# Performance work log

Hardware: AMD Instinct MI355X
Metric: run time of the kernel (lower is better)

Reference implementation:

```python
import jax, jax.numpy as jnp
from jax import lax
import numpy as np

H = 256

def _cell(x, h, c, wih, whh, bih, bhh):
    # PyTorch LSTMCell: gates ordered i, f, g, o
    g = x @ wih.T + bih + h @ whh.T + bhh
    i, f, gg, o = jnp.split(g, 4, axis=-1)
    c = jax.nn.sigmoid(f) * c + jax.nn.sigmoid(i) * jnp.tanh(gg)
    h = jax.nn.sigmoid(o) * jnp.tanh(c)
    return h, c


def setup_inputs() -> dict:
    key = jax.random.key(0)
    ks = iter(jax.random.split(key, 64))
    def lin(out_f, in_f):
        s = 1.0 / np.sqrt(in_f)
        w = jax.random.uniform(next(ks), (out_f, in_f), minval=-s, maxval=s, dtype=jnp.float32)
        b = jax.random.uniform(next(ks), (out_f,), minval=-s, maxval=s, dtype=jnp.float32)
        return w, b
    def cellp():
        s = 1.0 / np.sqrt(H)
        return tuple(jax.random.uniform(next(ks), sh, minval=-s, maxval=s, dtype=jnp.float32)
                     for sh in [(4 * H, H), (4 * H, H), (4 * H,), (4 * H,)])
    d = {}
    d['x'] = jax.random.normal(next(ks), (20, 256, 64, 64), dtype=jnp.float32)
    d['fc_en1_w'], d['fc_en1_b'] = lin(1024, 4096)
    d['fc_en2_w'], d['fc_en2_b'] = lin(H, 1024)
    for nm in ['en1', 'en2', 'en3', 'de1', 'de2', 'de3']:
        d[nm + '_wih'], d[nm + '_whh'], d[nm + '_bih'], d[nm + '_bhh'] = cellp()
    d['fc_de1_w'], d['fc_de1_b'] = lin(1024, H)
    d['fc_de2_w'], d['fc_de2_b'] = lin(4096, 1024)
    d['future_step'] = 10
    return d


def reference(x, fc_en1_w, fc_en1_b, fc_en2_w, fc_en2_b,
              en1_wih, en1_whh, en1_bih, en1_bhh,
              en2_wih, en2_whh, en2_bih, en2_bhh,
              en3_wih, en3_whh, en3_bih, en3_bhh,
              de1_wih, de1_whh, de1_bih, de1_bhh,
              de2_wih, de2_whh, de2_bih, de2_bhh,
              de3_wih, de3_whh, de3_bih, de3_bhh,
              fc_de1_w, fc_de1_b, fc_de2_w, fc_de2_b, future_step):
    seq, B = x.shape[0], x.shape[1]
    xf = x.reshape(seq, B, -1)  # (S, B, 4096)
    z0 = jnp.zeros((B, H), x.dtype)

    def enc_step(carry, xt):
        h1, c1, h2, c2, h3, c3 = carry
        z = jax.nn.relu(xt @ fc_en1_w.T + fc_en1_b)
        z = jax.nn.relu(z @ fc_en2_w.T + fc_en2_b)
        h1, c1 = _cell(z, h1, c1, en1_wih, en1_whh, en1_bih, en1_bhh)
        h2, c2 = _cell(h1, h2, c2, en2_wih, en2_whh, en2_bih, en2_bhh)
        h3, c3 = _cell(h2, h3, c3, en3_wih, en3_whh, en3_bih, en3_bhh)
        return (h1, c1, h2, c2, h3, c3), None

    enc_carry, _ = lax.scan(enc_step, (z0,) * 6, xf)
    h_e3 = enc_carry[4]

    def dec_step(carry, _):
        h1, c1, h2, c2, h3, c3 = carry
        h1, c1 = _cell(z0, h1, c1, de1_wih, de1_whh, de1_bih, de1_bhh)
        h2, c2 = _cell(h1, h2, c2, de2_wih, de2_whh, de2_bih, de2_bhh)
        h3, c3 = _cell(h2, h3, c3, de3_wih, de3_whh, de3_bih, de3_bhh)
        y = jax.nn.relu(h3 @ fc_de1_w.T + fc_de1_b)
        y = jnp.tanh(y @ fc_de2_w.T + fc_de2_b)
        return (h1, c1, h2, c2, h3, c3), y

    _, ys = lax.scan(dec_step, (h_e3, z0, z0, z0, z0, z0), None, length=future_step)
    return ys.reshape(future_step, B, 64, 64)
```

## Files before the change

### kernel.cpp

```cpp
#include <hip/hip_runtime.h>
#include <math.h>

static __device__ __forceinline__ float sigf(float v) { return 1.0f / (1.0f + expf(-v)); }

using s8v = __attribute__((ext_vector_type(8))) short;
using f4v = __attribute__((ext_vector_type(4))) float;

static __device__ __forceinline__ void splitf(float f, unsigned short& h, unsigned short& l) {
  unsigned u = __float_as_uint(f);
  unsigned short hb = (unsigned short)((u + 0x7FFFu + ((u >> 16) & 1u)) >> 16);
  float hf = __uint_as_float(((unsigned)hb) << 16);
  float lf = f - hf;
  unsigned ul = __float_as_uint(lf);
  unsigned short lb = (unsigned short)((ul + 0x7FFFu + ((ul >> 16) & 1u)) >> 16);
  h = hb; l = lb;
}

static __device__ __forceinline__ void splitf4(float4 a, uint2& hOut, uint2& lOut) {
  unsigned hxy, hzw;
  asm("v_cvt_pk_bf16_f32 %0, %1, %2" : "=v"(hxy) : "v"(a.x), "v"(a.y));
  asm("v_cvt_pk_bf16_f32 %0, %1, %2" : "=v"(hzw) : "v"(a.z), "v"(a.w));
  float hx = __uint_as_float(hxy << 16);
  float hy = __uint_as_float(hxy & 0xFFFF0000u);
  float hz = __uint_as_float(hzw << 16);
  float hw = __uint_as_float(hzw & 0xFFFF0000u);
  unsigned lxy, lzw;
  asm("v_cvt_pk_bf16_f32 %0, %1, %2" : "=v"(lxy) : "v"(a.x - hx), "v"(a.y - hy));
  asm("v_cvt_pk_bf16_f32 %0, %1, %2" : "=v"(lzw) : "v"(a.z - hz), "v"(a.w - hw));
  hOut.x = hxy; hOut.y = hzw;
  lOut.x = lxy; lOut.y = lzw;
}

__global__ __launch_bounds__(256) void wsplit(
    const float* __restrict__ W, unsigned short* __restrict__ WH,
    unsigned short* __restrict__ WL, int n4)
{
  int i = blockIdx.x * 256 + threadIdx.x;
  if (i < n4) {
    float4 v = ((const float4*)W)[i];
    ushort4 h, l;
    splitf(v.x, h.x, l.x); splitf(v.y, h.y, l.y);
    splitf(v.z, h.z, l.z); splitf(v.w, h.w, l.w);
    ((ushort4*)WH)[i] = h;
    ((ushort4*)WL)[i] = l;
  }
}

template <int OSPLIT>
__global__ __launch_bounds__(256) void gemm_sf(
    const float* __restrict__ A,
    const unsigned short* __restrict__ WH, const unsigned short* __restrict__ WL,
    const float* __restrict__ bias, float* __restrict__ C,
    unsigned short* __restrict__ OH, unsigned short* __restrict__ OL,
    int M, int N, int K, int act)
{
  __shared__ unsigned short AsH[128 * 40];
  __shared__ unsigned short AsL[128 * 40];
  __shared__ unsigned short WsH[64 * 40];
  __shared__ unsigned short WsL[64 * 40];

  const int t = threadIdx.x;
  const int w = t >> 6, lane = t & 63;
  const int lrow = lane & 15, lk = (lane >> 4) * 8;
  const int m0 = blockIdx.x * 128, n0 = blockIdx.y * 64;

  f4v acc[2][4];
#pragma unroll
  for (int i = 0; i < 2; ++i)
#pragma unroll
    for (int j = 0; j < 4; ++j) acc[i][j] = (f4v){0.f, 0.f, 0.f, 0.f};

  for (int k0 = 0; k0 < K; k0 += 32) {
#pragma unroll
    for (int i = 0; i < 4; ++i) {
      int v = i * 256 + t;
      int row = v >> 3, kq = (v & 7) << 2;
      float4 a = *(const float4*)(A + (size_t)(m0 + row) * K + k0 + kq);
      uint2 h2, l2;
      splitf4(a, h2, l2);
      *(uint2*)&AsH[row * 40 + kq] = h2;
      *(uint2*)&AsL[row * 40 + kq] = l2;
    }
    {
      int row = t >> 2, q = (t & 3) * 8;
      *(s8v*)&WsH[row * 40 + q] = *(const s8v*)(WH + (size_t)(n0 + row) * K + k0 + q);
      *(s8v*)&WsL[row * 40 + q] = *(const s8v*)(WL + (size_t)(n0 + row) * K + k0 + q);
    }
    __syncthreads();

    s8v aH[2], aL[2], bH[4], bL[4];
#pragma unroll
    for (int mt = 0; mt < 2; ++mt) {
      int r = (w * 32 + mt * 16 + lrow) * 40 + lk;
      aH[mt] = *(const s8v*)&AsH[r];
      aL[mt] = *(const s8v*)&AsL[r];
    }
#pragma unroll
    for (int nt = 0; nt < 4; ++nt) {
      int r = (nt * 16 + lrow) * 40 + lk;
      bH[nt] = *(const s8v*)&WsH[r];
      bL[nt] = *(const s8v*)&WsL[r];
    }
#pragma unroll
    for (int mt = 0; mt < 2; ++mt)
#pragma unroll
      for (int nt = 0; nt < 4; ++nt) {
        acc[mt][nt] = __builtin_amdgcn_mfma_f32_16x16x32_bf16(aH[mt], bH[nt], acc[mt][nt], 0, 0, 0);
        acc[mt][nt] = __builtin_amdgcn_mfma_f32_16x16x32_bf16(aH[mt], bL[nt], acc[mt][nt], 0, 0, 0);
        acc[mt][nt] = __builtin_amdgcn_mfma_f32_16x16x32_bf16(aL[mt], bH[nt], acc[mt][nt], 0, 0, 0);
      }
    __syncthreads();
  }

#pragma unroll
  for (int mt = 0; mt < 2; ++mt)
#pragma unroll
    for (int nt = 0; nt < 4; ++nt) {
      int gcol = n0 + nt * 16 + lrow;
      float bv = bias[gcol];
#pragma unroll
      for (int r = 0; r < 4; ++r) {
        int grow = m0 + w * 32 + mt * 16 + (lane >> 4) * 4 + r;
        float v = acc[mt][nt][r] + bv;
        if (act == 1) v = fmaxf(v, 0.f);
        else if (act == 2) v = tanhf(v);
        if (OSPLIT) {
          unsigned short h, l;
          splitf(v, h, l);
          OH[(size_t)grow * N + gcol] = h;
          OL[(size_t)grow * N + gcol] = l;
        } else {
          C[(size_t)grow * N + gcol] = v;
        }
      }
    }
}

template <int OSPLIT>
__global__ __launch_bounds__(256) void gemm_bb(
    const unsigned short* __restrict__ AH, const unsigned short* __restrict__ AL,
    const unsigned short* __restrict__ WH, const unsigned short* __restrict__ WL,
    const float* __restrict__ bias, float* __restrict__ C,
    unsigned short* __restrict__ OH, unsigned short* __restrict__ OL,
    int M, int N, int K, int act)
{
  __shared__ unsigned short AsH[128 * 40];
  __shared__ unsigned short AsL[128 * 40];
  __shared__ unsigned short WsH[64 * 40];
  __shared__ unsigned short WsL[64 * 40];

  const int t = threadIdx.x;
  const int w = t >> 6, lane = t & 63;
  const int lrow = lane & 15, lk = (lane >> 4) * 8;
  const int m0 = blockIdx.x * 128, n0 = blockIdx.y * 64;

  f4v acc[2][4];
#pragma unroll
  for (int i = 0; i < 2; ++i)
#pragma unroll
    for (int j = 0; j < 4; ++j) acc[i][j] = (f4v){0.f, 0.f, 0.f, 0.f};

  for (int k0 = 0; k0 < K; k0 += 32) {
#pragma unroll
    for (int i = 0; i < 2; ++i) {
      int v = i * 256 + t;
      int row = v >> 2, q = (v & 3) * 8;
      *(s8v*)&AsH[row * 40 + q] = *(const s8v*)(AH + (size_t)(m0 + row) * K + k0 + q);
      *(s8v*)&AsL[row * 40 + q] = *(const s8v*)(AL + (size_t)(m0 + row) * K + k0 + q);
    }
    {
      int row = t >> 2, q = (t & 3) * 8;
      *(s8v*)&WsH[row * 40 + q] = *(const s8v*)(WH + (size_t)(n0 + row) * K + k0 + q);
      *(s8v*)&WsL[row * 40 + q] = *(const s8v*)(WL + (size_t)(n0 + row) * K + k0 + q);
    }
    __syncthreads();

    s8v aH[2], aL[2], bH[4], bL[4];
#pragma unroll
    for (int mt = 0; mt < 2; ++mt) {
      int r = (w * 32 + mt * 16 + lrow) * 40 + lk;
      aH[mt] = *(const s8v*)&AsH[r];
      aL[mt] = *(const s8v*)&AsL[r];
    }
#pragma unroll
    for (int nt = 0; nt < 4; ++nt) {
      int r = (nt * 16 + lrow) * 40 + lk;
      bH[nt] = *(const s8v*)&WsH[r];
      bL[nt] = *(const s8v*)&WsL[r];
    }
#pragma unroll
    for (int mt = 0; mt < 2; ++mt)
#pragma unroll
      for (int nt = 0; nt < 4; ++nt) {
        acc[mt][nt] = __builtin_amdgcn_mfma_f32_16x16x32_bf16(aH[mt], bH[nt], acc[mt][nt], 0, 0, 0);
        acc[mt][nt] = __builtin_amdgcn_mfma_f32_16x16x32_bf16(aH[mt], bL[nt], acc[mt][nt], 0, 0, 0);
        acc[mt][nt] = __builtin_amdgcn_mfma_f32_16x16x32_bf16(aL[mt], bH[nt], acc[mt][nt], 0, 0, 0);
      }
    __syncthreads();
  }

#pragma unroll
  for (int mt = 0; mt < 2; ++mt)
#pragma unroll
    for (int nt = 0; nt < 4; ++nt) {
      int gcol = n0 + nt * 16 + lrow;
      float bv = bias[gcol];
#pragma unroll
      for (int r = 0; r < 4; ++r) {
        int grow = m0 + w * 32 + mt * 16 + (lane >> 4) * 4 + r;
        float v = acc[mt][nt][r] + bv;
        if (act == 1) v = fmaxf(v, 0.f);
        else if (act == 2) v = tanhf(v);
        if (OSPLIT) {
          unsigned short h, l;
          splitf(v, h, l);
          OH[(size_t)grow * N + gcol] = h;
          OL[(size_t)grow * N + gcol] = l;
        } else {
          C[(size_t)grow * N + gcol] = v;
        }
      }
    }
}

__global__ __launch_bounds__(256) void prep_pack(
    const float* __restrict__ wih, const float* __restrict__ whh,
    const float* __restrict__ bih, const float* __restrict__ bhh,
    float* __restrict__ wihP, float* __restrict__ whhP, float* __restrict__ bP)
{
  const int j = blockIdx.x, k = threadIdx.x;
  float4 a, c;
  a.x = wih[(0 * 256 + j) * 256 + k];
  a.y = wih[(1 * 256 + j) * 256 + k];
  a.z = wih[(2 * 256 + j) * 256 + k];
  a.w = wih[(3 * 256 + j) * 256 + k];
  *(float4*)&wihP[((size_t)j * 256 + k) * 4] = a;
  c.x = whh[(0 * 256 + j) * 256 + k];
  c.y = whh[(1 * 256 + j) * 256 + k];
  c.z = whh[(2 * 256 + j) * 256 + k];
  c.w = whh[(3 * 256 + j) * 256 + k];
  *(float4*)&whhP[((size_t)j * 256 + k) * 4] = c;
  if (k < 4) bP[j * 4 + k] = bih[k * 256 + j] + bhh[k * 256 + j];
}

__global__ __launch_bounds__(256) void transpose256(
    const float* __restrict__ in, float* __restrict__ out)
{
  const int t = blockIdx.x, c4 = blockIdx.y;
  const int r = threadIdx.x;
  float4 v = *(const float4*)(in + ((size_t)t * 256 + r) * 256 + c4 * 4);
  float* op = out + (size_t)t * 65536 + (size_t)(c4 * 4) * 256 + r;
  op[0]   = v.x;
  op[256] = v.y;
  op[512] = v.z;
  op[768] = v.w;
}

__global__ __launch_bounds__(256) void transpose256s(
    const float* __restrict__ in, unsigned short* __restrict__ outH,
    unsigned short* __restrict__ outL)
{
  const int t = blockIdx.x, c4 = blockIdx.y;
  const int r = threadIdx.x;
  float4 v = *(const float4*)(in + ((size_t)t * 256 + r) * 256 + c4 * 4);
  ushort4 h, l;
  splitf(v.x, h.x, l.x); splitf(v.y, h.y, l.y);
  splitf(v.z, h.z, l.z); splitf(v.w, h.w, l.w);
  size_t o = (size_t)t * 65536 + (size_t)(c4 * 4) * 256 + r;
  outH[o] = h.x; outH[o + 256] = h.y; outH[o + 512] = h.z; outH[o + 768] = h.w;
  outL[o] = l.x; outL[o + 256] = l.y; outL[o + 512] = l.z; outL[o + 768] = l.w;
}

struct CellSlot {
  const float* x;
  const float* wih;
  const float* whh;
  const float* bias;
  const float* hin;
  float* c;
  float* hout;
  float* hcopy;
  int hasx;
};
struct CellArgs { CellSlot s[3]; };

__global__ __launch_bounds__(512) void cell_multi(CellArgs args)
{
  __shared__ float part[4][64][4];
  const CellSlot S = args.s[blockIdx.x >> 8];
  const int inner = blockIdx.x & 255;
  const int jg = inner & 63, bg = inner >> 6;
  const int t = threadIdx.x;
  const int lane = t & 63;
  const int wave = t >> 6;
  const int jwv = wave & 3;
  const int kh = __builtin_amdgcn_readfirstlane(wave >> 2);
  const int b = bg * 64 + lane;

  const int jw = __builtin_amdgcn_readfirstlane(jg * 4 + jwv);
  const float4* wh = (const float4*)(S.whh + (size_t)jw * 1024) + kh * 128;
  const float4* wi = (const float4*)(S.wih + (size_t)jw * 1024) + kh * 128;
  const float* hcol = S.hin + (size_t)kh * 128 * 256 + b;

  float4 acc;
  if (kh == 0) acc = *(const float4*)(S.bias + jw * 4);
  else         acc = (float4){0.f, 0.f, 0.f, 0.f};

  if (S.hasx) {
    const float* xcol = S.x + (size_t)kh * 128 * 256 + b;
#pragma unroll 8
    for (int k = 0; k < 128; ++k) {
      const float hv = hcol[k * 256];
      const float4 wv = wh[k];
      acc.x = fmaf(hv, wv.x, acc.x);
      acc.y = fmaf(hv, wv.y, acc.y);
      acc.z = fmaf(hv, wv.z, acc.z);
      acc.w = fmaf(hv, wv.w, acc.w);
      const float xv = xcol[k * 256];
      const float4 vv = wi[k];
      acc.x = fmaf(xv, vv.x, acc.x);
      acc.y = fmaf(xv, vv.y, acc.y);
      acc.z = fmaf(xv, vv.z, acc.z);
      acc.w = fmaf(xv, vv.w, acc.w);
    }
  } else {
#pragma unroll 8
    for (int k = 0; k < 128; ++k) {
      const float hv = hcol[k * 256];
      const float4 wv = wh[k];
      acc.x = fmaf(hv, wv.x, acc.x);
      acc.y = fmaf(hv, wv.y, acc.y);
      acc.z = fmaf(hv, wv.z, acc.z);
      acc.w = fmaf(hv, wv.w, acc.w);
    }
  }

  if (kh == 1) *(float4*)&part[jwv][lane][0] = acc;
  __syncthreads();
  if (kh == 0) {
    const float4 p = *(const float4*)&part[jwv][lane][0];
    acc.x += p.x; acc.y += p.y; acc.z += p.z; acc.w += p.w;

    const int idx = jw * 256 + b;
    const float cold = S.c[idx];
    const float ig = sigf(acc.x), fg = sigf(acc.y);
    const float gg = tanhf(acc.z), og = sigf(acc.w);
    const float cn = fg * cold + ig * gg;
    const float hn = og * tanhf(cn);
    S.c[idx] = cn;
    S.hout[idx] = hn;
    if (S.hcopy) S.hcopy[idx] = hn;
  }
}


extern "C" void kernel_launch(void* const* d_in, const int* in_sizes, int n_in,
                              void* d_out, int out_size, void* d_ws, size_t ws_size,
                              hipStream_t stream)
{
  const float* x_in  = (const float*)d_in[0];
  const float* w_en1 = (const float*)d_in[1];
  const float* b_en1 = (const float*)d_in[2];
  const float* w_en2 = (const float*)d_in[3];
  const float* b_en2 = (const float*)d_in[4];
  const float* cw[6][4];
  for (int i = 0; i < 6; ++i)
    for (int j = 0; j < 4; ++j) cw[i][j] = (const float*)d_in[5 + i * 4 + j];
  const float* w_de1 = (const float*)d_in[29];
  const float* b_de1 = (const float*)d_in[30];
  const float* w_de2 = (const float*)d_in[31];
  const float* b_de2 = (const float*)d_in[32];
  float* out = (float*)d_out;

  float* fs   = (float*)d_ws;
  float* wihP = fs;
  float* whhP = wihP + 6 * 262144;
  float* bP   = whhP + 6 * 262144;
  float* hb   = bP + 6 * 1024;
  float* cb   = hb + 12 * 65536;
  float* H3T  = cb + 6 * 65536;
  float* z2   = H3T + 10 * 65536;
  float* z2T  = z2 + 1310720;
  unsigned short* us = (unsigned short*)(z2T + 1310720);
  unsigned short* WEN1H = us;              us += 4194304;
  unsigned short* WEN1L = us;              us += 4194304;
  unsigned short* WEN2H = us;              us += 262144;
  unsigned short* WEN2L = us;              us += 262144;
  unsigned short* WDE1H = us;              us += 262144;
  unsigned short* WDE1L = us;              us += 262144;
  unsigned short* WDE2H = us;              us += 4194304;
  unsigned short* WDE2L = us;              us += 4194304;
  unsigned short* Z1H   = us;              us += 5242880;
  unsigned short* Z1L   = us;              us += 5242880;
  unsigned short* H3H = Z1H;
  unsigned short* H3L = Z1H + 655360;
  unsigned short* Y1H = Z1H + 1310720;
  unsigned short* Y1L = Z1H + 1310720 + 2621440;

  for (int i = 0; i < 6; ++i)
    prep_pack<<<256, 256, 0, stream>>>(cw[i][0], cw[i][1], cw[i][2], cw[i][3],
                                       wihP + i * 262144, whhP + i * 262144,
                                       bP + i * 1024);
  wsplit<<<4096, 256, 0, stream>>>(w_en1, WEN1H, WEN1L, 1048576);
  wsplit<<<256, 256, 0, stream>>>(w_en2, WEN2H, WEN2L, 65536);
  wsplit<<<256, 256, 0, stream>>>(w_de1, WDE1H, WDE1L, 65536);
  wsplit<<<4096, 256, 0, stream>>>(w_de2, WDE2H, WDE2L, 1048576);
  hipMemsetAsync(hb, 0, (size_t)18 * 65536 * sizeof(float), stream);

  gemm_sf<1><<<dim3(40, 16), 256, 0, stream>>>(
      x_in, WEN1H, WEN1L, b_en1, nullptr, Z1H, Z1L, 5120, 1024, 4096, 1);
  gemm_bb<0><<<dim3(40, 4), 256, 0, stream>>>(
      Z1H, Z1L, WEN2H, WEN2L, b_en2, z2, nullptr, nullptr, 5120, 256, 1024, 1);
  transpose256<<<dim3(20, 64), 256, 0, stream>>>(z2, z2T);

  int pp[6] = {0, 0, 0, 0, 0, 0};
  auto HBuf = [&](int l, int p) { return hb + (size_t)(l * 2 + p) * 65536; };
  auto CBuf = [&](int l) { return cb + (size_t)l * 65536; };
  auto WI = [&](int l) { return wihP + (size_t)l * 262144; };
  auto WHp = [&](int l) { return whhP + (size_t)l * 262144; };
  auto BB = [&](int l) { return bP + (size_t)l * 1024; };

  for (int s = 0; s <= 21; ++s) {
    CellArgs a; int n = 0; int tog[3]; int nt = 0;
    if (s < 20) {
      a.s[n++] = {z2T + (size_t)s * 65536, WI(0), WHp(0), BB(0),
                  HBuf(0, pp[0]), CBuf(0), HBuf(0, pp[0] ^ 1), nullptr, 1};
      tog[nt++] = 0;
    }
    if (s >= 1 && s <= 20) {
      a.s[n++] = {HBuf(0, pp[0]), WI(1), WHp(1), BB(1),
                  HBuf(1, pp[1]), CBuf(1), HBuf(1, pp[1] ^ 1), nullptr, 1};
      tog[nt++] = 1;
    }
    if (s >= 2) {
      a.s[n++] = {HBuf(1, pp[1]), WI(2), WHp(2), BB(2),
                  HBuf(2, pp[2]), CBuf(2), HBuf(2, pp[2] ^ 1), nullptr, 1};
      tog[nt++] = 2;
    }
    cell_multi<<<n * 256, 512, 0, stream>>>(a);
    for (int i = 0; i < nt; ++i) pp[tog[i]] ^= 1;
  }

  for (int s = 0; s <= 11; ++s) {
    CellArgs a; int n = 0; int tog[3]; int nt = 0;
    if (s < 10) {
      const float* h1in = (s == 0) ? HBuf(2, pp[2]) : HBuf(3, pp[3]);
      a.s[n++] = {nullptr, WI(3), WHp(3), BB(3),
                  h1in, CBuf(3), HBuf(3, pp[3] ^ 1), nullptr, 0};
      tog[nt++] = 3;
    }
    if (s >= 1 && s <= 10) {
      a.s[n++] = {HBuf(3, pp[3]), WI(4), WHp(4), BB(4),
                  HBuf(4, pp[4]), CBuf(4), HBuf(4, pp[4] ^ 1), nullptr, 1};
      tog[nt++] = 4;
    }
    if (s >= 2) {
      a.s[n++] = {HBuf(4, pp[4]), WI(5), WHp(5), BB(5),
                  HBuf(5, pp[5]), CBuf(5), HBuf(5, pp[5] ^ 1),
                  H3T + (size_t)(s - 2) * 65536, 1};
      tog[nt++] = 5;
    }
    cell_multi<<<n * 256, 512, 0, stream>>>(a);
    for (int i = 0; i < nt; ++i) pp[tog[i]] ^= 1;
  }

  transpose256s<<<dim3(10, 64), 256, 0, stream>>>(H3T, H3H, H3L);
  gemm_bb<1><<<dim3(20, 16), 256, 0, stream>>>(
      H3H, H3L, WDE1H, WDE1L, b_de1, nullptr, Y1H, Y1L, 2560, 1024, 256, 1);
  gemm_bb<0><<<dim3(20, 64), 256, 0, stream>>>(
      Y1H, Y1L, WDE2H, WDE2L, b_de2, out, nullptr, nullptr, 2560, 4096, 1024, 2);

  (void)in_sizes; (void)n_in; (void)out_size; (void)ws_size;
}
```

Baseline: 854.7 us.

## Retile fp32-input GEMM to 64x128 and batch weight-prep kernel launches

The first encoder GEMM, which reads fp32 activations and splits them into bf16 hi/lo pairs, now uses 64-row by 128-column tiles instead of 128x64. Each fp32 activation element is therefore split fewer times across column blocks, while each wave keeps a wider strip of 8 accumulators. The six LSTM weight-pack launches are merged into one 2D-grid launch, and the four weight-split launches into one segmented launch, to cut launch overhead. The trade-off is more reads of the weight operand per tile, more registers per wave, and a different grid shape (80x8).

```diff
diff --git a/kernel.cpp b/kernel.cpp
--- a/kernel.cpp
+++ b/kernel.cpp
@@ -31,19 +31,26 @@
   lOut.x = lxy; lOut.y = lzw;
 }
 
-__global__ __launch_bounds__(256) void wsplit(
-    const float* __restrict__ W, unsigned short* __restrict__ WH,
-    unsigned short* __restrict__ WL, int n4)
-{
-  int i = blockIdx.x * 256 + threadIdx.x;
-  if (i < n4) {
-    float4 v = ((const float4*)W)[i];
-    ushort4 h, l;
-    splitf(v.x, h.x, l.x); splitf(v.y, h.y, l.y);
-    splitf(v.z, h.z, l.z); splitf(v.w, h.w, l.w);
-    ((ushort4*)WH)[i] = h;
-    ((ushort4*)WL)[i] = l;
-  }
+struct WsplitArgs {
+  const float* W[4];
+  unsigned short* WH[4];
+  unsigned short* WL[4];
+};
+__global__ __launch_bounds__(256) void wsplit4(WsplitArgs a)
+{
+  int blk = blockIdx.x;
+  int seg, base;
+  if (blk < 4096)      { seg = 0; base = blk; }
+  else if (blk < 4352) { seg = 1; base = blk - 4096; }
+  else if (blk < 4608) { seg = 2; base = blk - 4352; }
+  else                 { seg = 3; base = blk - 4608; }
+  int i = base * 256 + threadIdx.x;
+  float4 v = ((const float4*)a.W[seg])[i];
+  ushort4 h, l;
+  splitf(v.x, h.x, l.x); splitf(v.y, h.y, l.y);
+  splitf(v.z, h.z, l.z); splitf(v.w, h.w, l.w);
+  ((ushort4*)a.WH[seg])[i] = h;
+  ((ushort4*)a.WL[seg])[i] = l;
 }
 
 template <int OSPLIT>
@@ -54,25 +61,23 @@
     unsigned short* __restrict__ OH, unsigned short* __restrict__ OL,
     int M, int N, int K, int act)
 {
-  __shared__ unsigned short AsH[128 * 40];
-  __shared__ unsigned short AsL[128 * 40];
-  __shared__ unsigned short WsH[64 * 40];
-  __shared__ unsigned short WsL[64 * 40];
+  __shared__ unsigned short AsH[64 * 40];
+  __shared__ unsigned short AsL[64 * 40];
+  __shared__ unsigned short WsH[128 * 40];
+  __shared__ unsigned short WsL[128 * 40];
 
   const int t = threadIdx.x;
   const int w = t >> 6, lane = t & 63;
   const int lrow = lane & 15, lk = (lane >> 4) * 8;
-  const int m0 = blockIdx.x * 128, n0 = blockIdx.y * 64;
-
-  f4v acc[2][4];
-#pragma unroll
-  for (int i = 0; i < 2; ++i)
-#pragma unroll
-    for (int j = 0; j < 4; ++j) acc[i][j] = (f4v){0.f, 0.f, 0.f, 0.f};
+  const int m0 = blockIdx.x * 64, n0 = blockIdx.y * 128;
+
+  f4v acc[8];
+#pragma unroll
+  for (int j = 0; j < 8; ++j) acc[j] = (f4v){0.f, 0.f, 0.f, 0.f};
 
   for (int k0 = 0; k0 < K; k0 += 32) {
 #pragma unroll
-    for (int i = 0; i < 4; ++i) {
+    for (int i = 0; i < 2; ++i) {
       int v = i * 256 + t;
       int row = v >> 3, kq = (v & 7) << 2;
       float4 a = *(const float4*)(A + (size_t)(m0 + row) * K + k0 + kq);
@@ -80,6 +85,90 @@
       splitf4(a, h2, l2);
       *(uint2*)&AsH[row * 40 + kq] = h2;
       *(uint2*)&AsL[row * 40 + kq] = l2;
+    }
+#pragma unroll
+    for (int i = 0; i < 2; ++i) {
+      int v = i * 256 + t;
+      int row = v >> 2, q = (v & 3) * 8;
+      *(s8v*)&WsH[row * 40 + q] = *(const s8v*)(WH + (size_t)(n0 + row) * K + k0 + q);
+      *(s8v*)&WsL[row * 40 + q] = *(const s8v*)(WL + (size_t)(n0 + row) * K + k0 + q);
+    }
+    __syncthreads();
+
+    s8v aH, aL, bH[8], bL[8];
+    {
+      int r = (w * 16 + lrow) * 40 + lk;
+      aH = *(const s8v*)&AsH[r];
+      aL = *(const s8v*)&AsL[r];
+    }
+#pragma unroll
+    for (int nt = 0; nt < 8; ++nt) {
+      int r = (nt * 16 + lrow) * 40 + lk;
+      bH[nt] = *(const s8v*)&WsH[r];
+      bL[nt] = *(const s8v*)&WsL[r];
+    }
+#pragma unroll
+    for (int nt = 0; nt < 8; ++nt) {
+      acc[nt] = __builtin_amdgcn_mfma_f32_16x16x32_bf16(aH, bH[nt], acc[nt], 0, 0, 0);
+      acc[nt] = __builtin_amdgcn_mfma_f32_16x16x32_bf16(aH, bL[nt], acc[nt], 0, 0, 0);
+      acc[nt] = __builtin_amdgcn_mfma_f32_16x16x32_bf16(aL, bH[nt], acc[nt], 0, 0, 0);
+    }
+    __syncthreads();
+  }
+
+#pragma unroll
+  for (int nt = 0; nt < 8; ++nt) {
+    int gcol = n0 + nt * 16 + lrow;
+    float bv = bias[gcol];
+#pragma unroll
+    for (int r = 0; r < 4; ++r) {
+      int grow = m0 + w * 16 + (lane >> 4) * 4 + r;
+      float v = acc[nt][r] + bv;
+      if (act == 1) v = fmaxf(v, 0.f);
+      else if (act == 2) v = tanhf(v);
+      if (OSPLIT) {
+        unsigned short h, l;
+        splitf(v, h, l);
+        OH[(size_t)grow * N + gcol] = h;
+        OL[(size_t)grow * N + gcol] = l;
+      } else {
+        C[(size_t)grow * N + gcol] = v;
+      }
+    }
+  }
+}
+
+template <int OSPLIT>
+__global__ __launch_bounds__(256) void gemm_bb(
+    const unsigned short* __restrict__ AH, const unsigned short* __restrict__ AL,
+    const unsigned short* __restrict__ WH, const unsigned short* __restrict__ WL,
+    const float* __restrict__ bias, float* __restrict__ C,
+    unsigned short* __restrict__ OH, unsigned short* __restrict__ OL,
+    int M, int N, int K, int act)
+{
+  __shared__ unsigned short AsH[128 * 40];
+  __shared__ unsigned short AsL[128 * 40];
+  __shared__ unsigned short WsH[64 * 40];
+  __shared__ unsigned short WsL[64 * 40];
+
+  const int t = threadIdx.x;
+  const int w = t >> 6, lane = t & 63;
+  const int lrow = lane & 15, lk = (lane >> 4) * 8;
+  const int m0 = blockIdx.x * 128, n0 = blockIdx.y * 64;
+
+  f4v acc[2][4];
+#pragma unroll
+  for (int i = 0; i < 2; ++i)
+#pragma unroll
+    for (int j = 0; j < 4; ++j) acc[i][j] = (f4v){0.f, 0.f, 0.f, 0.f};
+
+  for (int k0 = 0; k0 < K; k0 += 32) {
+#pragma unroll
+    for (int i = 0; i < 2; ++i) {
+      int v = i * 256 + t;
+      int row = v >> 2, q = (v & 3) * 8;
+      *(s8v*)&AsH[row * 40 + q] = *(const s8v*)(AH + (size_t)(m0 + row) * K + k0 + q);
+      *(s8v*)&AsL[row * 40 + q] = *(const s8v*)(AL + (size_t)(m0 + row) * K + k0 + q);
     }
     {
       int row = t >> 2, q = (t & 3) * 8;
@@ -136,111 +225,36 @@
     }
 }
 
-template <int OSPLIT>
-__global__ __launch_bounds__(256) void gemm_bb(
-    const unsigned short* __restrict__ AH, const unsigned short* __restrict__ AL,
-    const unsigned short* __restrict__ WH, const unsigned short* __restrict__ WL,
-    const float* __restrict__ bias, float* __restrict__ C,
-    unsigned short* __restrict__ OH, unsigned short* __restrict__ OL,
-    int M, int N, int K, int act)
-{
-  __shared__ unsigned short AsH[128 * 40];
-  __shared__ unsigned short AsL[128 * 40];
-  __shared__ unsigned short WsH[64 * 40];
-  __shared__ unsigned short WsL[64 * 40];
-
-  const int t = threadIdx.x;
-  const int w = t >> 6, lane = t & 63;
-  const int lrow = lane & 15, lk = (lane >> 4) * 8;
-  const int m0 = blockIdx.x * 128, n0 = blockIdx.y * 64;
-
-  f4v acc[2][4];
-#pragma unroll
-  for (int i = 0; i < 2; ++i)
-#pragma unroll
-    for (int j = 0; j < 4; ++j) acc[i][j] = (f4v){0.f, 0.f, 0.f, 0.f};
-
-  for (int k0 = 0; k0 < K; k0 += 32) {
-#pragma unroll
-    for (int i = 0; i < 2; ++i) {
-      int v = i * 256 + t;
-      int row = v >> 2, q = (v & 3) * 8;
-      *(s8v*)&AsH[row * 40 + q] = *(const s8v*)(AH + (size_t)(m0 + row) * K + k0 + q);
-      *(s8v*)&AsL[row * 40 + q] = *(const s8v*)(AL + (size_t)(m0 + row) * K + k0 + q);
-    }
-    {
-      int row = t >> 2, q = (t & 3) * 8;
-      *(s8v*)&WsH[row * 40 + q] = *(const s8v*)(WH + (size_t)(n0 + row) * K + k0 + q);
-      *(s8v*)&WsL[row * 40 + q] = *(const s8v*)(WL + (size_t)(n0 + row) * K + k0 + q);
-    }
-    __syncthreads();
-
-    s8v aH[2], aL[2], bH[4], bL[4];
-#pragma unroll
-    for (int mt = 0; mt < 2; ++mt) {
-      int r = (w * 32 + mt * 16 + lrow) * 40 + lk;
-      aH[mt] = *(const s8v*)&AsH[r];
-      aL[mt] = *(const s8v*)&AsL[r];
-    }
-#pragma unroll
-    for (int nt = 0; nt < 4; ++nt) {
-      int r = (nt * 16 + lrow) * 40 + lk;
-      bH[nt] = *(const s8v*)&WsH[r];
-      bL[nt] = *(const s8v*)&WsL[r];
-    }
-#pragma unroll
-    for (int mt = 0; mt < 2; ++mt)
-#pragma unroll
-      for (int nt = 0; nt < 4; ++nt) {
-        acc[mt][nt] = __builtin_amdgcn_mfma_f32_16x16x32_bf16(aH[mt], bH[nt], acc[mt][nt], 0, 0, 0);
-        acc[mt][nt] = __builtin_amdgcn_mfma_f32_16x16x32_bf16(aH[mt], bL[nt], acc[mt][nt], 0, 0, 0);
-        acc[mt][nt] = __builtin_amdgcn_mfma_f32_16x16x32_bf16(aL[mt], bH[nt], acc[mt][nt], 0, 0, 0);
-      }
-    __syncthreads();
-  }
-
-#pragma unroll
-  for (int mt = 0; mt < 2; ++mt)
-#pragma unroll
-    for (int nt = 0; nt < 4; ++nt) {
-      int gcol = n0 + nt * 16 + lrow;
-      float bv = bias[gcol];
-#pragma unroll
-      for (int r = 0; r < 4; ++r) {
-        int grow = m0 + w * 32 + mt * 16 + (lane >> 4) * 4 + r;
-        float v = acc[mt][nt][r] + bv;
-        if (act == 1) v = fmaxf(v, 0.f);
-        else if (act == 2) v = tanhf(v);
-        if (OSPLIT) {
-          unsigned short h, l;
-          splitf(v, h, l);
-          OH[(size_t)grow * N + gcol] = h;
-          OL[(size_t)grow * N + gcol] = l;
-        } else {
-          C[(size_t)grow * N + gcol] = v;
-        }
-      }
-    }
-}
-
-__global__ __launch_bounds__(256) void prep_pack(
-    const float* __restrict__ wih, const float* __restrict__ whh,
-    const float* __restrict__ bih, const float* __restrict__ bhh,
-    float* __restrict__ wihP, float* __restrict__ whhP, float* __restrict__ bP)
-{
+struct PrepArgs {
+  const float* wih[6];
+  const float* whh[6];
+  const float* bih[6];
+  const float* bhh[6];
+  float* wihP;
+  float* whhP;
+  float* bP;
+};
+__global__ __launch_bounds__(256) void prep_pack6(PrepArgs a)
+{
+  const int l = blockIdx.y;
   const int j = blockIdx.x, k = threadIdx.x;
-  float4 a, c;
-  a.x = wih[(0 * 256 + j) * 256 + k];
-  a.y = wih[(1 * 256 + j) * 256 + k];
-  a.z = wih[(2 * 256 + j) * 256 + k];
-  a.w = wih[(3 * 256 + j) * 256 + k];
-  *(float4*)&wihP[((size_t)j * 256 + k) * 4] = a;
+  const float* wih = a.wih[l];
+  const float* whh = a.whh[l];
+  float* wihP = a.wihP + (size_t)l * 262144;
+  float* whhP = a.whhP + (size_t)l * 262144;
+  float4 v, c;
+  v.x = wih[(0 * 256 + j) * 256 + k];
+  v.y = wih[(1 * 256 + j) * 256 + k];
+  v.z = wih[(2 * 256 + j) * 256 + k];
+  v.w = wih[(3 * 256 + j) * 256 + k];
+  *(float4*)&wihP[((size_t)j * 256 + k) * 4] = v;
   c.x = whh[(0 * 256 + j) * 256 + k];
   c.y = whh[(1 * 256 + j) * 256 + k];
   c.z = whh[(2 * 256 + j) * 256 + k];
   c.w = whh[(3 * 256 + j) * 256 + k];
   *(float4*)&whhP[((size_t)j * 256 + k) * 4] = c;
-  if (k < 4) bP[j * 4 + k] = bih[k * 256 + j] + bhh[k * 256 + j];
+  if (k < 4)
+    a.bP[l * 1024 + j * 4 + k] = a.bih[l][k * 256 + j] + a.bhh[l][k * 256 + j];
 }
 
 __global__ __launch_bounds__(256) void transpose256(
@@ -397,17 +411,23 @@
   unsigned short* Y1H = Z1H + 1310720;
   unsigned short* Y1L = Z1H + 1310720 + 2621440;
 
-  for (int i = 0; i < 6; ++i)
-    prep_pack<<<256, 256, 0, stream>>>(cw[i][0], cw[i][1], cw[i][2], cw[i][3],
-                                       wihP + i * 262144, whhP + i * 262144,
-                                       bP + i * 1024);
-  wsplit<<<4096, 256, 0, stream>>>(w_en1, WEN1H, WEN1L, 1048576);
-  wsplit<<<256, 256, 0, stream>>>(w_en2, WEN2H, WEN2L, 65536);
-  wsplit<<<256, 256, 0, stream>>>(w_de1, WDE1H, WDE1L, 65536);
-  wsplit<<<4096, 256, 0, stream>>>(w_de2, WDE2H, WDE2L, 1048576);
+  PrepArgs pa;
+  for (int i = 0; i < 6; ++i) {
+    pa.wih[i] = cw[i][0]; pa.whh[i] = cw[i][1];
+    pa.bih[i] = cw[i][2]; pa.bhh[i] = cw[i][3];
+  }
+  pa.wihP = wihP; pa.whhP = whhP; pa.bP = bP;
+  prep_pack6<<<dim3(256, 6), 256, 0, stream>>>(pa);
+
+  WsplitArgs wa;
+  wa.W[0] = w_en1; wa.WH[0] = WEN1H; wa.WL[0] = WEN1L;
+  wa.W[1] = w_en2; wa.WH[1] = WEN2H; wa.WL[1] = WEN2L;
+  wa.W[2] = w_de1; wa.WH[2] = WDE1H; wa.WL[2] = WDE1L;
+  wa.W[3] = w_de2; wa.WH[3] = WDE2H; wa.WL[3] = WDE2L;
+  wsplit4<<<8704, 256, 0, stream>>>(wa);
   hipMemsetAsync(hb, 0, (size_t)18 * 65536 * sizeof(float), stream);
 
-  gemm_sf<1><<<dim3(40, 16), 256, 0, stream>>>(
+  gemm_sf<1><<<dim3(80, 8), 256, 0, stream>>>(
       x_in, WEN1H, WEN1L, b_en1, nullptr, Z1H, Z1L, 5120, 1024, 4096, 1);
   gemm_bb<0><<<dim3(40, 4), 256, 0, stream>>>(
       Z1H, Z1L, WEN2H, WEN2L, b_en2, z2, nullptr, nullptr, 5120, 256, 1024, 1);
```

After: 875.6 us. +2.4%, slower.
